# Kernel optimization log

Hardware: AMD Instinct MI355X
Metric: run time of the kernel (lower is better)

The kernel has to match this reference:

```python
import jax, jax.numpy as jnp
import numpy as np
from jax import lax

GRID_N = 80
C_FEAT = 128
HID = 256
NLAYERS = 12


def _make_grid_mesh(n):
    xs = np.linspace(-0.9, 0.9, n, dtype=np.float32)
    X, Y = np.meshgrid(xs, xs, indexing='xy')
    verts = np.stack([X.ravel(), Y.ravel(), np.zeros(n * n, np.float32)], 1)
    idx = np.arange(n * n).reshape(n, n)
    a = idx[:-1, :-1].ravel(); b = idx[:-1, 1:].ravel()
    c = idx[1:, :-1].ravel(); d = idx[1:, 1:].ravel()
    faces = np.concatenate([np.stack([a, b, c], 1), np.stack([b, d, c], 1)], 0)
    return verts, faces.astype(np.int64)


def _edges_and_inv(faces):
    F = faces.shape[0]
    e = np.concatenate([faces[:, [0, 1]], faces[:, [1, 2]], faces[:, [2, 0]]], 0)
    e = np.sort(e, 1)
    edges, inv = np.unique(e, axis=0, return_inverse=True)
    inv = inv.reshape(-1)
    return edges.astype(np.int32), inv[:F], inv[F:2 * F], inv[2 * F:]


def _subdivide_faces(faces, V):
    # new vertex k is midpoint of unique edge k, placed at index V + k
    edges, i01, i12, i20 = _edges_and_inv(faces)
    m01 = V + i01; m12 = V + i12; m20 = V + i20
    v0, v1, v2 = faces[:, 0], faces[:, 1], faces[:, 2]
    nf = np.concatenate([np.stack([v0, m01, m20], 1), np.stack([v1, m12, m01], 1),
                         np.stack([v2, m20, m12], 1), np.stack([m01, m12, m20], 1)], 0)
    return edges, nf


def _topology():
    verts0, f1 = _make_grid_mesh(GRID_N)
    V1 = verts0.shape[0]
    edges1, f2 = _subdivide_faces(f1, V1)
    V2 = V1 + edges1.shape[0]
    edges2, f3 = _subdivide_faces(f2, V2)
    V3 = V2 + edges2.shape[0]
    edges3 = _edges_and_inv(f3)[0]
    return verts0, edges1, edges2, edges3, V3


def _vert_align(feat, verts):
    # feat [C,H,W]; sample bilinearly at vertex (x,y) in [-1,1], align_corners, zero padding
    C, H, W = feat.shape
    fx = (verts[:, 0] + 1.0) * 0.5 * (W - 1)
    fy = (verts[:, 1] + 1.0) * 0.5 * (H - 1)
    x0 = jnp.floor(fx); y0 = jnp.floor(fy)
    wx = fx - x0; wy = fy - y0
    x0i = x0.astype(jnp.int32); y0i = y0.astype(jnp.int32)
    fT = jnp.transpose(feat, (1, 2, 0))  # [H,W,C]

    def samp(yi, xi):
        valid = ((yi >= 0) & (yi < H) & (xi >= 0) & (xi < W)).astype(feat.dtype)
        v = fT[jnp.clip(yi, 0, H - 1), jnp.clip(xi, 0, W - 1)]
        return v * valid[:, None]

    return (samp(y0i, x0i) * ((1 - wy) * (1 - wx))[:, None]
            + samp(y0i, x0i + 1) * ((1 - wy) * wx)[:, None]
            + samp(y0i + 1, x0i) * (wy * (1 - wx))[:, None]
            + samp(y0i + 1, x0i + 1) * (wy * wx)[:, None])


def _gconv(x, e0, e1, w, b):
    # pytorch3d GraphConv: w0(x) + sum_{j in N(i)} w1(x_j), undirected edges
    h0 = x @ w[0] + b[0]
    h1 = x @ w[1] + b[1]
    agg = jnp.zeros_like(h0).at[e0].add(h1[e1]).at[e1].add(h1[e0])
    return h0 + agg


def _stage(feat, edges, w_in, b_in, w_h, b_h, w_out, b_out):
    e0, e1 = edges[:, 0], edges[:, 1]
    x = _gconv(feat, e0, e1, w_in, b_in)

    def body(xc, p):
        return _gconv(xc, e0, e1, p[0], p[1]), None

    x, _ = lax.scan(body, x, (w_h, b_h))
    coords = _gconv(x, e0, e1, w_out, b_out)
    return x, coords


def _subdiv(f, edges):
    # SubdivideMeshes feature/vertex rule: append edge midpoints
    return jnp.concatenate([f, 0.5 * (f[edges[:, 0]] + f[edges[:, 1]])], 0)


def setup_inputs() -> dict:
    key = jax.random.key(0)
    ks = jax.random.split(key, 16)
    verts0, edges1, edges2, edges3, V3 = _topology()

    def pw(k, din, dout, L=None):
        shape = (L, 2, din, dout) if L else (2, din, dout)
        return jax.random.normal(k, shape, dtype=jnp.float32) / np.float32(np.sqrt(7.0 * din))

    din2 = C_FEAT + HID
    inp = {
        'conv64': jax.random.normal(ks[0], (C_FEAT, 56, 56), jnp.float32),
        'conv128': jax.random.normal(ks[1], (C_FEAT, 28, 28), jnp.float32),
        'conv256': jax.random.normal(ks[2], (C_FEAT, 14, 14), jnp.float32),
        'verts0': jnp.asarray(verts0),
        'edges1': jnp.asarray(edges1), 'edges2': jnp.asarray(edges2), 'edges3': jnp.asarray(edges3),
        'w_in1': pw(ks[3], C_FEAT, HID), 'b_in1': jnp.zeros((2, HID), jnp.float32),
        'w_h1': pw(ks[4], HID, HID, NLAYERS), 'b_h1': jnp.zeros((NLAYERS, 2, HID), jnp.float32),
        'w_out1': pw(ks[5], HID, 3), 'b_out1': jnp.zeros((2, 3), jnp.float32),
        'w_in2': pw(ks[6], din2, HID), 'b_in2': jnp.zeros((2, HID), jnp.float32),
        'w_h2': pw(ks[7], HID, HID, NLAYERS), 'b_h2': jnp.zeros((NLAYERS, 2, HID), jnp.float32),
        'w_out2': pw(ks[8], HID, 3), 'b_out2': jnp.zeros((2, 3), jnp.float32),
        'w_in3': pw(ks[9], din2, HID), 'b_in3': jnp.zeros((2, HID), jnp.float32),
        'w_h3': pw(ks[10], HID, HID, NLAYERS), 'b_h3': jnp.zeros((NLAYERS, 2, HID), jnp.float32),
        'w_out3': pw(ks[11], HID, 3), 'b_out3': jnp.zeros((2, 3), jnp.float32),
    }
    return inp


def reference(conv64, conv128, conv256, verts0,
              w_in1, b_in1, w_h1, b_h1, w_out1, b_out1,
              w_in2, b_in2, w_h2, b_h2, w_out2, b_out2,
              w_in3, b_in3, w_h3, b_h3, w_out3, b_out3,
              edges1, edges2, edges3):
    # stage 1: vert_align on conv64 + 14 graph convs -> coords
    x, c1 = _stage(_vert_align(conv64, verts0), edges1, w_in1, b_in1, w_h1, b_h1, w_out1, b_out1)
    v2 = _subdiv(c1, edges1)
    h2 = _subdiv(x, edges1)
    f2 = jnp.concatenate([_vert_align(conv128, v2), h2], 1)
    x, c2 = _stage(f2, edges2, w_in2, b_in2, w_h2, b_h2, w_out2, b_out2)
    v3 = _subdiv(c2, edges2)
    h3 = _subdiv(x, edges2)
    f3 = jnp.concatenate([_vert_align(conv256, v3), h3], 1)
    _, c3 = _stage(f3, edges3, w_in3, b_in3, w_h3, b_h3, w_out3, b_out3)
    return c3
```

## Files before the change

kernel.cpp:

```cpp
#include <hip/hip_runtime.h>
#include <utility>

#define HID 256

typedef __attribute__((ext_vector_type(8))) short bf16x8;
typedef __attribute__((ext_vector_type(4))) float f32x4;
typedef __attribute__((ext_vector_type(4))) unsigned short us4;
typedef __attribute__((ext_vector_type(4))) unsigned uint4v;

constexpr size_t MAXN3 = 100489;
constexpr size_t MAXE3 = 300200;

constexpr size_t OFF_IN1 = 0;
constexpr size_t OFF_IN2 = OFF_IN1 + 2 * 256 * 128;
constexpr size_t OFF_IN3 = OFF_IN2 + 2 * 256 * 384;
constexpr size_t OFF_H1  = OFF_IN3 + 2 * 256 * 384;
constexpr size_t OFF_H2  = OFF_H1 + 24 * 256 * 256;
constexpr size_t OFF_H3  = OFF_H2 + 24 * 256 * 256;
constexpr size_t WT_TOTAL = OFF_H3 + 24 * 256 * 256;

__device__ __attribute__((aligned(16))) unsigned g_A [MAXN3 * 256];
__device__ __attribute__((aligned(16))) unsigned g_B [MAXN3 * 256];
__device__ __attribute__((aligned(16))) unsigned g_G [MAXN3 * 256];
__device__ __attribute__((aligned(16))) unsigned g_D [MAXN3 * 256];
__device__ __attribute__((aligned(16))) unsigned g_VA[MAXN3 * 128];
__device__ float g_C0[MAXN3 * 3];
__device__ float g_C2[MAXN3 * 3];
__device__ float g_Vv[MAXN3 * 3];
__device__ float g_T [56 * 56 * 128];
__device__ __attribute__((aligned(16))) unsigned short g_Wth[WT_TOTAL];
__device__ __attribute__((aligned(16))) unsigned short g_Wtl[WT_TOTAL];
__device__ int g_deg   [MAXN3];
__device__ int g_rowptr[MAXN3 + 1];
__device__ int g_cursor[MAXN3];
__device__ int g_adj   [2 * MAXE3];
__device__ int g_bsum  [128];

__device__ inline float rec(unsigned u) {
  return __uint_as_float(u & 0xffff0000u) + __uint_as_float(u << 16);
}
__device__ inline unsigned pck(float f) {
  unsigned u = __float_as_uint(f);
  unsigned hi = u & 0xffff0000u;
  unsigned lo = __float_as_uint(f - __uint_as_float(hi)) >> 16;
  return hi | (lo & 0xffffu);
}

#define GLOAD16(g, l)                                                       \
  __builtin_amdgcn_global_load_lds(                                        \
      (const __attribute__((address_space(1))) unsigned*)(g),              \
      (__attribute__((address_space(3))) unsigned*)(l), 16, 0, 0)

__global__ __launch_bounds__(256) void k_wtrans(const float* __restrict__ W,
                                                unsigned short* __restrict__ Oh,
                                                unsigned short* __restrict__ Ol,
                                                int K) {
  __shared__ float Ls[64][65];
  int ktb = blockIdx.x, cb = blockIdx.y, mat = blockIdx.z;
  int nktb = gridDim.x;
  const float* Wm = W + (size_t)mat * K * 256;
  int t = threadIdx.x;
#pragma unroll
  for (int i = 0; i < 16; ++i) {
    int idx = i * 256 + t;
    int kk = idx >> 6, cc = idx & 63;
    Ls[kk][cc] = Wm[(size_t)(ktb * 64 + kk) * 256 + cb * 64 + cc];
  }
  __syncthreads();
  size_t tb = ((size_t)(mat * 4 + cb) * nktb + ktb) * 4096;
#pragma unroll
  for (int i = 0; i < 2; ++i) {
    int c = t * 2 + i;
    int n = c >> 3, sp = c & 7;
    int kbase = (sp ^ (n & 7)) * 8;
    unsigned short hb[8], lb[8];
#pragma unroll
    for (int j = 0; j < 8; ++j) {
      float v = Ls[kbase + j][n];
      unsigned u = __float_as_uint(v);
      unsigned short hi = (unsigned short)(u >> 16);
      float hf = __uint_as_float(u & 0xffff0000u);
      hb[j] = hi;
      lb[j] = (unsigned short)(__float_as_uint(v - hf) >> 16);
    }
    *(us4*)(Oh + tb + c * 8)     = (us4){hb[0], hb[1], hb[2], hb[3]};
    *(us4*)(Oh + tb + c * 8 + 4) = (us4){hb[4], hb[5], hb[6], hb[7]};
    *(us4*)(Ol + tb + c * 8)     = (us4){lb[0], lb[1], lb[2], lb[3]};
    *(us4*)(Ol + tb + c * 8 + 4) = (us4){lb[4], lb[5], lb[6], lb[7]};
  }
}


__global__ __launch_bounds__(256) void k_count(const int* __restrict__ edges,
                                               int* __restrict__ deg, int E) {
  int e = blockIdx.x * blockDim.x + threadIdx.x;
  if (e >= E) return;
  atomicAdd(&deg[edges[2 * e + 0]], 1);
  atomicAdd(&deg[edges[2 * e + 1]], 1);
}

__global__ __launch_bounds__(256) void k_scan_part(const int* __restrict__ deg,
                                                   int* __restrict__ bsum, int N) {
  __shared__ int s[256];
  int t = threadIdx.x;
  int base = blockIdx.x * 1024 + t * 4;
  int v = 0;
#pragma unroll
  for (int i = 0; i < 4; ++i) {
    int idx = base + i;
    if (idx < N) v += deg[idx];
  }
  s[t] = v;
  __syncthreads();
  for (int off = 128; off > 0; off >>= 1) {
    if (t < off) s[t] += s[t + off];
    __syncthreads();
  }
  if (t == 0) bsum[blockIdx.x] = s[0];
}

__global__ __launch_bounds__(128) void k_scan_top(int* __restrict__ bsum, int nb) {
  __shared__ int s[128];
  int t = threadIdx.x;
  s[t] = (t < nb) ? bsum[t] : 0;
  __syncthreads();
  for (int off = 1; off < 128; off <<= 1) {
    int v = (t >= off) ? s[t - off] : 0;
    __syncthreads();
    s[t] += v;
    __syncthreads();
  }
  if (t < nb) bsum[t] = (t == 0) ? 0 : s[t - 1];
}

__global__ __launch_bounds__(256) void k_scan_write(const int* __restrict__ deg,
                                                    const int* __restrict__ bsum,
                                                    int* __restrict__ rowptr,
                                                    int* __restrict__ cursor, int N) {
  __shared__ int s[256];
  int t = threadIdx.x;
  int base = blockIdx.x * 1024;
  int d[4];
  int local = 0;
#pragma unroll
  for (int i = 0; i < 4; ++i) {
    int idx = base + t * 4 + i;
    d[i] = (idx < N) ? deg[idx] : 0;
    local += d[i];
  }
  s[t] = local;
  __syncthreads();
  for (int off = 1; off < 256; off <<= 1) {
    int v = (t >= off) ? s[t - off] : 0;
    __syncthreads();
    s[t] += v;
    __syncthreads();
  }
  int run = bsum[blockIdx.x] + s[t] - local;
#pragma unroll
  for (int i = 0; i < 4; ++i) {
    int idx = base + t * 4 + i;
    if (idx < N) {
      rowptr[idx] = run;
      cursor[idx] = run;
    }
    run += d[i];
  }
  if (blockIdx.x == gridDim.x - 1 && t == 255) rowptr[N] = run;
}

__global__ __launch_bounds__(256) void k_fill(const int* __restrict__ edges,
                                              int* __restrict__ cursor,
                                              int* __restrict__ adj, int E) {
  int e = blockIdx.x * blockDim.x + threadIdx.x;
  if (e >= E) return;
  int a = edges[2 * e + 0];
  int b = edges[2 * e + 1];
  adj[atomicAdd(&cursor[a], 1)] = b;
  adj[atomicAdd(&cursor[b], 1)] = a;
}


__global__ __launch_bounds__(128) void k_transpose(const float* __restrict__ in,
                                                   float* __restrict__ out, int HW) {
  int p = blockIdx.x;
  int c = threadIdx.x;
  if (p < HW) out[(size_t)p * 128 + c] = in[(size_t)c * HW + p];
}

__global__ __launch_bounds__(128) void k_vert_align(const float* __restrict__ fT,
                                                    const float* __restrict__ verts,
                                                    unsigned* __restrict__ out,
                                                    int N, int H, int W) {
  int v = blockIdx.x;
  if (v >= N) return;
  int c = threadIdx.x;
  float vx = verts[(size_t)v * 3 + 0];
  float vy = verts[(size_t)v * 3 + 1];
  float fx = (vx + 1.f) * 0.5f * (float)(W - 1);
  float fy = (vy + 1.f) * 0.5f * (float)(H - 1);
  float x0f = floorf(fx), y0f = floorf(fy);
  float wx = fx - x0f, wy = fy - y0f;
  int x0 = (int)x0f, y0 = (int)y0f;
  float acc = 0.f;
#pragma unroll
  for (int dy = 0; dy < 2; ++dy) {
#pragma unroll
    for (int dx = 0; dx < 2; ++dx) {
      int yi = y0 + dy, xi = x0 + dx;
      bool valid = (yi >= 0) && (yi < H) && (xi >= 0) && (xi < W);
      int yc = min(max(yi, 0), H - 1);
      int xc = min(max(xi, 0), W - 1);
      float val = fT[((size_t)yc * W + xc) * 128 + c];
      float wgt = (dy ? wy : 1.f - wy) * (dx ? wx : 1.f - wx);
      acc += valid ? val * wgt : 0.f;
    }
  }
  out[(size_t)v * 128 + c] = pck(acc);
}

template <int CH>
__global__ __launch_bounds__(256) void k_gather(const int* __restrict__ rowptr,
                                                const int* __restrict__ adj,
                                                const unsigned* __restrict__ X,
                                                unsigned* __restrict__ G, int N) {
  int idx = blockIdx.x * blockDim.x + threadIdx.x;
  int v = idx / (CH / 4);
  if (v >= N) return;
  int c = (idx % (CH / 4)) * 4;
  float a0 = 0.f, a1 = 0.f, a2 = 0.f, a3 = 0.f;
  int lo = rowptr[v], hi = rowptr[v + 1];
  for (int i = lo; i < hi; ++i) {
    uint4 h = *(const uint4*)(X + (size_t)adj[i] * CH + c);
    a0 += rec(h.x); a1 += rec(h.y); a2 += rec(h.z); a3 += rec(h.w);
  }
  uint4 o;
  o.x = pck(a0); o.y = pck(a1); o.z = pck(a2); o.w = pck(a3);
  *(uint4*)(G + (size_t)v * CH + c) = o;
}

struct Panels {
  const unsigned* p[4];
  int ks[4];
  int ld[4];
};

#define SWZ(row, slot) (((row) * 64) + (((slot) ^ ((row) & 7)) * 8))

__device__ inline bf16x8 as_bf(uint4v v) {
  union { uint4v u; bf16x8 b; } x;
  x.u = v;
  return x.b;
}

__global__ __launch_bounds__(256) void k_layer(
    Panels pd, int Kmm,
    const unsigned short* __restrict__ w0h, const unsigned short* __restrict__ w0l,
    const unsigned short* __restrict__ w1h, const unsigned short* __restrict__ w1l,
    int Kw,
    const float* __restrict__ b0, const float* __restrict__ b1,
    const int* __restrict__ deg,
    unsigned* __restrict__ Y, int N) {
  __shared__ __attribute__((aligned(16))) unsigned X_lds[128 * 64];
  __shared__ __attribute__((aligned(16))) unsigned short Wh_lds[4096];
  __shared__ __attribute__((aligned(16))) unsigned short Wl_lds[4096];
  int tid = threadIdx.x;
  int lane = tid & 63;
  int wid = tid >> 6;
  int wm = wid & 1, wn = wid >> 1;

  int nrt = (N + 127) >> 7;
  int total = nrt * 4;
  int flat = blockIdx.x;
  int rowtile, colblk;
  if ((flat & ~31) + 32 <= total) {
    int sub = flat & 31;
    rowtile = (flat >> 5) * 8 + (sub & 7);
    colblk = sub >> 3;
  } else {
    rowtile = flat >> 2;
    colblk = flat & 3;
  }
  int row0 = rowtile * 128;
  int col0 = colblk * 64;
  int nktbw = Kw >> 6;

  f32x4 acc[4][2];
#pragma unroll
  for (int m = 0; m < 4; ++m)
#pragma unroll
    for (int n = 0; n < 2; ++n) acc[m][n] = (f32x4){0.f, 0.f, 0.f, 0.f};

  for (int kt = 0; kt < Kmm; kt += 64) {
    int pi = (kt >= pd.ks[1]) + (kt >= pd.ks[2]) + (kt >= pd.ks[3]);
    const unsigned* base = pd.p[pi];
    int ld = pd.ld[pi];
    int koff = kt - pd.ks[pi];
#pragma unroll
    for (int i = 0; i < 8; ++i) {
      int inst = wid * 8 + i;
      int row = inst * 4 + (lane >> 4);
      int j = lane & 15;
      int vc = min(row0 + row, N - 1);
      const unsigned* src = base + (size_t)vc * ld + koff + ((j ^ (row & 15)) << 2);
      GLOAD16(src, &X_lds[inst * 256]);
    }
    const unsigned short* th;
    const unsigned short* tl;
    {
      int ktb = (kt < Kw) ? (kt >> 6) : ((kt - Kw) >> 6);
      const unsigned short* mh = (kt < Kw) ? w0h : w1h;
      const unsigned short* ml = (kt < Kw) ? w0l : w1l;
      size_t tb = ((size_t)(colblk * nktbw + ktb)) * 4096;
      th = mh + tb;
      tl = ml + tb;
    }
#pragma unroll
    for (int i = 0; i < 2; ++i) {
      int inst = wid * 2 + i;
      GLOAD16(th + inst * 512 + lane * 8, &Wh_lds[inst * 512]);
      GLOAD16(tl + inst * 512 + lane * 8, &Wl_lds[inst * 512]);
    }
    __syncthreads();
#pragma unroll
    for (int ks = 0; ks < 2; ++ks) {
      int slot = ks * 4 + (lane >> 4);
      bf16x8 ah[4], al[4];
#pragma unroll
      for (int m = 0; m < 4; ++m) {
        int row = wm * 64 + m * 16 + (lane & 15);
        int rx = row & 15;
        const unsigned* xp = X_lds + row * 64;
        uint4 u0 = *(const uint4*)(xp + (((2 * slot) ^ rx) << 2));
        uint4 u1 = *(const uint4*)(xp + (((2 * slot + 1) ^ rx) << 2));
        uint4v hv, lv;
        hv.x = __builtin_amdgcn_perm(u0.y, u0.x, 0x07060302u);
        hv.y = __builtin_amdgcn_perm(u0.w, u0.z, 0x07060302u);
        hv.z = __builtin_amdgcn_perm(u1.y, u1.x, 0x07060302u);
        hv.w = __builtin_amdgcn_perm(u1.w, u1.z, 0x07060302u);
        lv.x = __builtin_amdgcn_perm(u0.y, u0.x, 0x05040100u);
        lv.y = __builtin_amdgcn_perm(u0.w, u0.z, 0x05040100u);
        lv.z = __builtin_amdgcn_perm(u1.y, u1.x, 0x05040100u);
        lv.w = __builtin_amdgcn_perm(u1.w, u1.z, 0x05040100u);
        ah[m] = as_bf(hv);
        al[m] = as_bf(lv);
      }
      bf16x8 bh[2], bl[2];
#pragma unroll
      for (int n = 0; n < 2; ++n) {
        int nr = wn * 32 + n * 16 + (lane & 15);
        int wi = SWZ(nr, slot);
        bh[n] = *(const bf16x8*)&Wh_lds[wi];
        bl[n] = *(const bf16x8*)&Wl_lds[wi];
      }
#pragma unroll
      for (int m = 0; m < 4; ++m)
#pragma unroll
        for (int n = 0; n < 2; ++n) {
          f32x4 c = acc[m][n];
          c = __builtin_amdgcn_mfma_f32_16x16x32_bf16(al[m], bh[n], c, 0, 0, 0);
          c = __builtin_amdgcn_mfma_f32_16x16x32_bf16(ah[m], bl[n], c, 0, 0, 0);
          c = __builtin_amdgcn_mfma_f32_16x16x32_bf16(ah[m], bh[n], c, 0, 0, 0);
          acc[m][n] = c;
        }
    }
    __syncthreads();
  }

#pragma unroll
  for (int m = 0; m < 4; ++m) {
    int rbase = row0 + wm * 64 + m * 16 + (lane >> 4) * 4;
    float dv[4];
#pragma unroll
    for (int r = 0; r < 4; ++r)
      dv[r] = (rbase + r < N) ? (float)deg[rbase + r] : 0.f;
#pragma unroll
    for (int n = 0; n < 2; ++n) {
      int col = col0 + wn * 32 + n * 16 + (lane & 15);
      float bb0 = b0[col], bb1 = b1[col];
      f32x4 v = acc[m][n];
#pragma unroll
      for (int r = 0; r < 4; ++r) {
        int row = rbase + r;
        if (row < N)
          Y[(size_t)row * HID + col] = pck(v[r] + bb0 + dv[r] * bb1);
      }
    }
  }
}

__global__ __launch_bounds__(256) void k_rowdot6(const unsigned* __restrict__ X,
                                                 const float* __restrict__ W,
                                                 const float* __restrict__ b,
                                                 float* __restrict__ Y0,
                                                 float* __restrict__ Y1, int N) {
  int gid = blockIdx.x * blockDim.x + threadIdx.x;
  int row = gid >> 6;
  int lane = threadIdx.x & 63;
  if (row >= N) return;
  uint4 xv = ((const uint4*)(X + (size_t)row * HID))[lane];
  float s[6] = {0.f, 0.f, 0.f, 0.f, 0.f, 0.f};
#pragma unroll
  for (int k = 0; k < 4; ++k) {
    float x = rec((&xv.x)[k]);
    int kk = lane * 4 + k;
#pragma unroll
    for (int j = 0; j < 3; ++j) {
      s[j]     += x * W[kk * 3 + j];
      s[3 + j] += x * W[768 + kk * 3 + j];
    }
  }
#pragma unroll
  for (int off = 32; off > 0; off >>= 1)
#pragma unroll
    for (int j = 0; j < 6; ++j) s[j] += __shfl_down(s[j], off);
  if (lane == 0) {
#pragma unroll
    for (int j = 0; j < 3; ++j) {
      Y0[(size_t)row * 3 + j] = s[j] + b[j];
      Y1[(size_t)row * 3 + j] = s[3 + j] + b[3 + j];
    }
  }
}

__global__ __launch_bounds__(256) void k_scatter3(const int* __restrict__ edges,
                                                  const float* __restrict__ H,
                                                  float* __restrict__ OUT, int E) {
  int e = blockIdx.x * blockDim.x + threadIdx.x;
  if (e >= E) return;
  int a = edges[(size_t)e * 2 + 0];
  int b = edges[(size_t)e * 2 + 1];
#pragma unroll
  for (int k = 0; k < 3; ++k) {
    atomicAdd(&OUT[(size_t)a * 3 + k], H[(size_t)b * 3 + k]);
    atomicAdd(&OUT[(size_t)b * 3 + k], H[(size_t)a * 3 + k]);
  }
}

__global__ __launch_bounds__(256) void k_subdiv3(const float* __restrict__ c,
                                                 const int* __restrict__ edges,
                                                 float* __restrict__ v, int N, int E) {
  int i = blockIdx.x * blockDim.x + threadIdx.x;
  if (i >= N + E) return;
  if (i < N) {
#pragma unroll
    for (int k = 0; k < 3; ++k) v[(size_t)i * 3 + k] = c[(size_t)i * 3 + k];
  } else {
    int e = i - N;
    int a = edges[(size_t)e * 2 + 0];
    int b = edges[(size_t)e * 2 + 1];
#pragma unroll
    for (int k = 0; k < 3; ++k)
      v[(size_t)i * 3 + k] = 0.5f * (c[(size_t)a * 3 + k] + c[(size_t)b * 3 + k]);
  }
}

__global__ __launch_bounds__(256) void k_subdiv_feat(const unsigned* __restrict__ x,
                                                     const int* __restrict__ edges,
                                                     unsigned* __restrict__ out, int N, int E) {
  int idx = blockIdx.x * blockDim.x + threadIdx.x;
  int v = idx >> 6;
  if (v >= N + E) return;
  int c = (threadIdx.x & 63) * 4;
  uint4 r;
  if (v < N) {
    r = *(const uint4*)(x + (size_t)v * HID + c);
  } else {
    int e = v - N;
    int a = edges[(size_t)e * 2 + 0];
    int b = edges[(size_t)e * 2 + 1];
    uint4 xa = *(const uint4*)(x + (size_t)a * HID + c);
    uint4 xb = *(const uint4*)(x + (size_t)b * HID + c);
    r.x = pck(0.5f * (rec(xa.x) + rec(xb.x)));
    r.y = pck(0.5f * (rec(xa.y) + rec(xb.y)));
    r.z = pck(0.5f * (rec(xa.z) + rec(xb.z)));
    r.w = pck(0.5f * (rec(xa.w) + rec(xb.w)));
  }
  *(uint4*)(out + (size_t)v * HID + c) = r;
}


extern "C" void kernel_launch(void* const* d_in, const int* in_sizes, int n_in,
                              void* d_out, int out_size, void* d_ws, size_t ws_size,
                              hipStream_t stream) {
  const float* conv64  = (const float*)d_in[0];
  const float* conv128 = (const float*)d_in[1];
  const float* conv256 = (const float*)d_in[2];
  const float* verts0  = (const float*)d_in[3];
  const int*   edges1  = (const int*)d_in[4];
  const int*   edges2  = (const int*)d_in[5];
  const int*   edges3  = (const int*)d_in[6];
  const float* w_in1 = (const float*)d_in[7],  *b_in1 = (const float*)d_in[8];
  const float* w_h1  = (const float*)d_in[9],  *b_h1  = (const float*)d_in[10];
  const float* w_out1= (const float*)d_in[11], *b_out1= (const float*)d_in[12];
  const float* w_in2 = (const float*)d_in[13], *b_in2 = (const float*)d_in[14];
  const float* w_h2  = (const float*)d_in[15], *b_h2  = (const float*)d_in[16];
  const float* w_out2= (const float*)d_in[17], *b_out2= (const float*)d_in[18];
  const float* w_in3 = (const float*)d_in[19], *b_in3 = (const float*)d_in[20];
  const float* w_h3  = (const float*)d_in[21], *b_h3  = (const float*)d_in[22];
  const float* w_out3= (const float*)d_in[23], *b_out3= (const float*)d_in[24];

  const int N1 = in_sizes[3] / 3;
  const int E1 = in_sizes[4] / 2;
  const int E2 = in_sizes[5] / 2;
  const int E3 = in_sizes[6] / 2;
  const int N2 = N1 + E1;
  const int N3 = N2 + E2;
  if ((size_t)N3 > MAXN3 || (size_t)E3 > MAXE3) return;

  unsigned *A, *B, *G, *D, *VA;
  float *C0, *C2, *Vv, *T;
  unsigned short *Wth, *Wtl;
  int *deg, *rowptr, *cursor, *adj, *bsum;
  hipGetSymbolAddress((void**)&A,  HIP_SYMBOL(g_A));
  hipGetSymbolAddress((void**)&B,  HIP_SYMBOL(g_B));
  hipGetSymbolAddress((void**)&G,  HIP_SYMBOL(g_G));
  hipGetSymbolAddress((void**)&D,  HIP_SYMBOL(g_D));
  hipGetSymbolAddress((void**)&VA, HIP_SYMBOL(g_VA));
  hipGetSymbolAddress((void**)&C0, HIP_SYMBOL(g_C0));
  hipGetSymbolAddress((void**)&C2, HIP_SYMBOL(g_C2));
  hipGetSymbolAddress((void**)&Vv, HIP_SYMBOL(g_Vv));
  hipGetSymbolAddress((void**)&T,  HIP_SYMBOL(g_T));
  hipGetSymbolAddress((void**)&Wth, HIP_SYMBOL(g_Wth));
  hipGetSymbolAddress((void**)&Wtl, HIP_SYMBOL(g_Wtl));
  hipGetSymbolAddress((void**)&deg,    HIP_SYMBOL(g_deg));
  hipGetSymbolAddress((void**)&rowptr, HIP_SYMBOL(g_rowptr));
  hipGetSymbolAddress((void**)&cursor, HIP_SYMBOL(g_cursor));
  hipGetSymbolAddress((void**)&adj,    HIP_SYMBOL(g_adj));
  hipGetSymbolAddress((void**)&bsum,   HIP_SYMBOL(g_bsum));

  k_wtrans<<<dim3(2, 4, 2),  256, 0, stream>>>(w_in1, Wth + OFF_IN1, Wtl + OFF_IN1, 128);
  k_wtrans<<<dim3(6, 4, 2),  256, 0, stream>>>(w_in2, Wth + OFF_IN2, Wtl + OFF_IN2, 384);
  k_wtrans<<<dim3(6, 4, 2),  256, 0, stream>>>(w_in3, Wth + OFF_IN3, Wtl + OFF_IN3, 384);
  k_wtrans<<<dim3(4, 4, 24), 256, 0, stream>>>(w_h1,  Wth + OFF_H1,  Wtl + OFF_H1,  256);
  k_wtrans<<<dim3(4, 4, 24), 256, 0, stream>>>(w_h2,  Wth + OFF_H2,  Wtl + OFF_H2,  256);
  k_wtrans<<<dim3(4, 4, 24), 256, 0, stream>>>(w_h3,  Wth + OFF_H3,  Wtl + OFF_H3,  256);

  const int BIG = 0x7fffffff;

  auto layerGrid = [](int N) { return dim3((unsigned)(((N + 127) / 128) * 4)); };

  auto build_csr = [&](const int* edges, int E, int N) {
    hipMemsetAsync(deg, 0, (size_t)N * sizeof(int), stream);
    k_count<<<(E + 255) / 256, 256, 0, stream>>>(edges, deg, E);
    int nb = (N + 1023) / 1024;
    k_scan_part<<<nb, 256, 0, stream>>>(deg, bsum, N);
    k_scan_top<<<1, 128, 0, stream>>>(bsum, nb);
    k_scan_write<<<nb, 256, 0, stream>>>(deg, bsum, rowptr, cursor, N);
    k_fill<<<(E + 255) / 256, 256, 0, stream>>>(edges, cursor, adj, E);
  };

  auto gconv_hidden = [&](size_t offH, const float* bh, int N) {
    unsigned* X = A; unsigned* Y = B;
    for (int l = 0; l < 12; ++l) {
      const unsigned short* w0h = Wth + offH + (size_t)(2 * l + 0) * 65536;
      const unsigned short* w0l = Wtl + offH + (size_t)(2 * l + 0) * 65536;
      const unsigned short* w1h = Wth + offH + (size_t)(2 * l + 1) * 65536;
      const unsigned short* w1l = Wtl + offH + (size_t)(2 * l + 1) * 65536;
      const float* b0 = bh + (size_t)l * 2 * HID;
      const float* b1 = b0 + HID;
      k_gather<256><<<((size_t)N * 64 + 255) / 256, 256, 0, stream>>>(rowptr, adj, X, G, N);
      Panels pd = {{X, G, nullptr, nullptr}, {0, 256, BIG, BIG}, {256, 256, 0, 0}};
      k_layer<<<layerGrid(N), 256, 0, stream>>>(pd, 512, w0h, w0l, w1h, w1l, 256,
                                                b0, b1, deg, Y, N);
      std::swap(X, Y);
    }
  };

  auto gconv_out = [&](const unsigned* X, const float* wo, const float* bo,
                       float* Cdst, const int* edges, int E, int N) {
    k_rowdot6<<<((size_t)N * 64 + 255) / 256, 256, 0, stream>>>(X, wo, bo, Cdst, C2, N);
    k_scatter3<<<(E + 255) / 256, 256, 0, stream>>>(edges, C2, Cdst, E);
  };

  build_csr(edges1, E1, N1);
  k_transpose<<<56 * 56, 128, 0, stream>>>(conv64, T, 56 * 56);
  k_vert_align<<<N1, 128, 0, stream>>>(T, verts0, VA, N1, 56, 56);
  k_gather<128><<<((size_t)N1 * 32 + 255) / 256, 256, 0, stream>>>(rowptr, adj, VA, G, N1);
  {
    Panels pd = {{VA, G, nullptr, nullptr}, {0, 128, BIG, BIG}, {128, 128, 0, 0}};
    k_layer<<<layerGrid(N1), 256, 0, stream>>>(pd, 256,
        Wth + OFF_IN1, Wtl + OFF_IN1, Wth + OFF_IN1 + 32768, Wtl + OFF_IN1 + 32768, 128,
        b_in1, b_in1 + HID, deg, A, N1);
  }
  gconv_hidden(OFF_H1, b_h1, N1);
  gconv_out(A, w_out1, b_out1, C0, edges1, E1, N1);
  k_subdiv3<<<(N2 + 255) / 256, 256, 0, stream>>>(C0, edges1, Vv, N1, E1);
  k_subdiv_feat<<<((size_t)N2 * 64 + 255) / 256, 256, 0, stream>>>(A, edges1, D, N1, E1);

  build_csr(edges2, E2, N2);
  k_transpose<<<28 * 28, 128, 0, stream>>>(conv128, T, 28 * 28);
  k_vert_align<<<N2, 128, 0, stream>>>(T, Vv, VA, N2, 28, 28);
  k_gather<128><<<((size_t)N2 * 32 + 255) / 256, 256, 0, stream>>>(rowptr, adj, VA, G, N2);
  k_gather<256><<<((size_t)N2 * 64 + 255) / 256, 256, 0, stream>>>(rowptr, adj, D, B, N2);
  {
    const size_t m0 = OFF_IN2, m1 = OFF_IN2 + (size_t)256 * 384;
    Panels pd = {{VA, D, G, B}, {0, 128, 384, 512}, {128, 256, 128, 256}};
    k_layer<<<layerGrid(N2), 256, 0, stream>>>(pd, 768,
        Wth + m0, Wtl + m0, Wth + m1, Wtl + m1, 384,
        b_in2, b_in2 + HID, deg, A, N2);
  }
  gconv_hidden(OFF_H2, b_h2, N2);
  gconv_out(A, w_out2, b_out2, C0, edges2, E2, N2);
  k_subdiv3<<<(N3 + 255) / 256, 256, 0, stream>>>(C0, edges2, Vv, N2, E2);
  k_subdiv_feat<<<((size_t)N3 * 64 + 255) / 256, 256, 0, stream>>>(A, edges2, D, N2, E2);

  build_csr(edges3, E3, N3);
  k_transpose<<<14 * 14, 128, 0, stream>>>(conv256, T, 14 * 14);
  k_vert_align<<<N3, 128, 0, stream>>>(T, Vv, VA, N3, 14, 14);
  k_gather<128><<<((size_t)N3 * 32 + 255) / 256, 256, 0, stream>>>(rowptr, adj, VA, G, N3);
  k_gather<256><<<((size_t)N3 * 64 + 255) / 256, 256, 0, stream>>>(rowptr, adj, D, B, N3);
  {
    const size_t m0 = OFF_IN3, m1 = OFF_IN3 + (size_t)256 * 384;
    Panels pd = {{VA, D, G, B}, {0, 128, 384, 512}, {128, 256, 128, 256}};
    k_layer<<<layerGrid(N3), 256, 0, stream>>>(pd, 768,
        Wth + m0, Wtl + m0, Wth + m1, Wtl + m1, 384,
        b_in3, b_in3 + HID, deg, A, N3);
  }
  gconv_hidden(OFF_H3, b_h3, N3);
  float* OUT = (float*)d_out;
  k_rowdot6<<<((size_t)N3 * 64 + 255) / 256, 256, 0, stream>>>(A, w_out3, b_out3, OUT, C2, N3);
  k_scatter3<<<(E3 + 255) / 256, 256, 0, stream>>>(edges3, C2, OUT, E3);
}
```

Measured before the change: 4.577 ms.

## Store activations as separate bf16 hi/lo planes instead of interleaved words

Activation buffers used to hold packed 32-bit words (bf16 hi and lo halves interleaved). They are now split into two separate planes of unsigned short, across the gather, vert_align, subdivision, rowdot and layer kernels. In the GEMM kernel this removes the per-fragment perm instructions that de-interleaved hi and lo from LDS, since each plane can be loaded directly as a bf16x8 operand. The cost is twice as many global and LDS load streams per tile and separate write streams in every producer kernel, with the same total byte traffic.

Measured after the change: 4.221 ms. 7.8% less time.

```diff
diff --git a/kernel.cpp b/kernel.cpp
--- a/kernel.cpp
+++ b/kernel.cpp
@@ -6,7 +6,7 @@
 typedef __attribute__((ext_vector_type(8))) short bf16x8;
 typedef __attribute__((ext_vector_type(4))) float f32x4;
 typedef __attribute__((ext_vector_type(4))) unsigned short us4;
-typedef __attribute__((ext_vector_type(4))) unsigned uint4v;
+typedef __attribute__((ext_vector_type(8))) unsigned short us8;
 
 constexpr size_t MAXN3 = 100489;
 constexpr size_t MAXE3 = 300200;
@@ -19,11 +19,16 @@
 constexpr size_t OFF_H3  = OFF_H2 + 24 * 256 * 256;
 constexpr size_t WT_TOTAL = OFF_H3 + 24 * 256 * 256;
 
-__device__ __attribute__((aligned(16))) unsigned g_A [MAXN3 * 256];
-__device__ __attribute__((aligned(16))) unsigned g_B [MAXN3 * 256];
-__device__ __attribute__((aligned(16))) unsigned g_G [MAXN3 * 256];
-__device__ __attribute__((aligned(16))) unsigned g_D [MAXN3 * 256];
-__device__ __attribute__((aligned(16))) unsigned g_VA[MAXN3 * 128];
+__device__ __attribute__((aligned(16))) unsigned short g_Ah[MAXN3 * 256];
+__device__ __attribute__((aligned(16))) unsigned short g_Al[MAXN3 * 256];
+__device__ __attribute__((aligned(16))) unsigned short g_Bh[MAXN3 * 256];
+__device__ __attribute__((aligned(16))) unsigned short g_Bl[MAXN3 * 256];
+__device__ __attribute__((aligned(16))) unsigned short g_Gh[MAXN3 * 256];
+__device__ __attribute__((aligned(16))) unsigned short g_Gl[MAXN3 * 256];
+__device__ __attribute__((aligned(16))) unsigned short g_Dh[MAXN3 * 256];
+__device__ __attribute__((aligned(16))) unsigned short g_Dl[MAXN3 * 256];
+__device__ __attribute__((aligned(16))) unsigned short g_VAh[MAXN3 * 128];
+__device__ __attribute__((aligned(16))) unsigned short g_VAl[MAXN3 * 128];
 __device__ float g_C0[MAXN3 * 3];
 __device__ float g_C2[MAXN3 * 3];
 __device__ float g_Vv[MAXN3 * 3];
@@ -36,20 +41,20 @@
 __device__ int g_adj   [2 * MAXE3];
 __device__ int g_bsum  [128];
 
-__device__ inline float rec(unsigned u) {
-  return __uint_as_float(u & 0xffff0000u) + __uint_as_float(u << 16);
-}
-__device__ inline unsigned pck(float f) {
+__device__ inline float b2f(unsigned short h) {
+  return __uint_as_float((unsigned)h << 16);
+}
+__device__ inline void fsplit(float f, unsigned short& h, unsigned short& l) {
   unsigned u = __float_as_uint(f);
-  unsigned hi = u & 0xffff0000u;
-  unsigned lo = __float_as_uint(f - __uint_as_float(hi)) >> 16;
-  return hi | (lo & 0xffffu);
+  h = (unsigned short)(u >> 16);
+  float hf = __uint_as_float(u & 0xffff0000u);
+  l = (unsigned short)(__float_as_uint(f - hf) >> 16);
 }
 
 #define GLOAD16(g, l)                                                       \
   __builtin_amdgcn_global_load_lds(                                        \
-      (const __attribute__((address_space(1))) unsigned*)(g),              \
-      (__attribute__((address_space(3))) unsigned*)(l), 16, 0, 0)
+      (const __attribute__((address_space(1))) unsigned*)(const void*)(g), \
+      (__attribute__((address_space(3))) unsigned*)(void*)(l), 16, 0, 0)
 
 __global__ __launch_bounds__(256) void k_wtrans(const float* __restrict__ W,
                                                 unsigned short* __restrict__ Oh,
@@ -77,11 +82,10 @@
 #pragma unroll
     for (int j = 0; j < 8; ++j) {
       float v = Ls[kbase + j][n];
-      unsigned u = __float_as_uint(v);
-      unsigned short hi = (unsigned short)(u >> 16);
-      float hf = __uint_as_float(u & 0xffff0000u);
+      unsigned short hi, lo;
+      fsplit(v, hi, lo);
       hb[j] = hi;
-      lb[j] = (unsigned short)(__float_as_uint(v - hf) >> 16);
+      lb[j] = lo;
     }
     *(us4*)(Oh + tb + c * 8)     = (us4){hb[0], hb[1], hb[2], hb[3]};
     *(us4*)(Oh + tb + c * 8 + 4) = (us4){hb[4], hb[5], hb[6], hb[7]};
@@ -190,7 +194,8 @@
 
 __global__ __launch_bounds__(128) void k_vert_align(const float* __restrict__ fT,
                                                     const float* __restrict__ verts,
-                                                    unsigned* __restrict__ out,
+                                                    unsigned short* __restrict__ oh,
+                                                    unsigned short* __restrict__ ol,
                                                     int N, int H, int W) {
   int v = blockIdx.x;
   if (v >= N) return;
@@ -216,42 +221,53 @@
       acc += valid ? val * wgt : 0.f;
     }
   }
-  out[(size_t)v * 128 + c] = pck(acc);
+  unsigned short h, l;
+  fsplit(acc, h, l);
+  oh[(size_t)v * 128 + c] = h;
+  ol[(size_t)v * 128 + c] = l;
 }
 
 template <int CH>
 __global__ __launch_bounds__(256) void k_gather(const int* __restrict__ rowptr,
                                                 const int* __restrict__ adj,
-                                                const unsigned* __restrict__ X,
-                                                unsigned* __restrict__ G, int N) {
+                                                const unsigned short* __restrict__ Xh,
+                                                const unsigned short* __restrict__ Xl,
+                                                unsigned short* __restrict__ Gh,
+                                                unsigned short* __restrict__ Gl, int N) {
+  constexpr int TPV = CH / 8;
   int idx = blockIdx.x * blockDim.x + threadIdx.x;
-  int v = idx / (CH / 4);
+  int v = idx / TPV;
   if (v >= N) return;
-  int c = (idx % (CH / 4)) * 4;
-  float a0 = 0.f, a1 = 0.f, a2 = 0.f, a3 = 0.f;
+  int c = (idx % TPV) * 8;
+  float a[8] = {};
   int lo = rowptr[v], hi = rowptr[v + 1];
   for (int i = lo; i < hi; ++i) {
-    uint4 h = *(const uint4*)(X + (size_t)adj[i] * CH + c);
-    a0 += rec(h.x); a1 += rec(h.y); a2 += rec(h.z); a3 += rec(h.w);
-  }
-  uint4 o;
-  o.x = pck(a0); o.y = pck(a1); o.z = pck(a2); o.w = pck(a3);
-  *(uint4*)(G + (size_t)v * CH + c) = o;
+    size_t base = (size_t)adj[i] * CH + c;
+    us8 h = *(const us8*)(Xh + base);
+    us8 l = *(const us8*)(Xl + base);
+#pragma unroll
+    for (int j = 0; j < 8; ++j) a[j] += b2f(h[j]) + b2f(l[j]);
+  }
+  us8 oh, ol;
+#pragma unroll
+  for (int j = 0; j < 8; ++j) {
+    unsigned short hh, ll;
+    fsplit(a[j], hh, ll);
+    oh[j] = hh;
+    ol[j] = ll;
+  }
+  *(us8*)(Gh + (size_t)v * CH + c) = oh;
+  *(us8*)(Gl + (size_t)v * CH + c) = ol;
 }
 
 struct Panels {
-  const unsigned* p[4];
+  const unsigned short* ph[4];
+  const unsigned short* pl[4];
   int ks[4];
   int ld[4];
 };
 
-#define SWZ(row, slot) (((row) * 64) + (((slot) ^ ((row) & 7)) * 8))
-
-__device__ inline bf16x8 as_bf(uint4v v) {
-  union { uint4v u; bf16x8 b; } x;
-  x.u = v;
-  return x.b;
-}
+#define SWZ(row, slot) (((row) * 64) + (((slot) ^ ((row) & 7)) << 3))
 
 __global__ __launch_bounds__(256) void k_layer(
     Panels pd, int Kmm,
@@ -260,8 +276,9 @@
     int Kw,
     const float* __restrict__ b0, const float* __restrict__ b1,
     const int* __restrict__ deg,
-    unsigned* __restrict__ Y, int N) {
-  __shared__ __attribute__((aligned(16))) unsigned X_lds[128 * 64];
+    unsigned short* __restrict__ Yh, unsigned short* __restrict__ Yl, int N) {
+  __shared__ __attribute__((aligned(16))) unsigned short Xh_lds[128 * 64];
+  __shared__ __attribute__((aligned(16))) unsigned short Xl_lds[128 * 64];
   __shared__ __attribute__((aligned(16))) unsigned short Wh_lds[4096];
   __shared__ __attribute__((aligned(16))) unsigned short Wl_lds[4096];
   int tid = threadIdx.x;
@@ -293,17 +310,18 @@
 
   for (int kt = 0; kt < Kmm; kt += 64) {
     int pi = (kt >= pd.ks[1]) + (kt >= pd.ks[2]) + (kt >= pd.ks[3]);
-    const unsigned* base = pd.p[pi];
+    const unsigned short* bph = pd.ph[pi];
+    const unsigned short* bpl = pd.pl[pi];
     int ld = pd.ld[pi];
     int koff = kt - pd.ks[pi];
 #pragma unroll
-    for (int i = 0; i < 8; ++i) {
-      int inst = wid * 8 + i;
-      int row = inst * 4 + (lane >> 4);
-      int j = lane & 15;
-      int vc = min(row0 + row, N - 1);
-      const unsigned* src = base + (size_t)vc * ld + koff + ((j ^ (row & 15)) << 2);
-      GLOAD16(src, &X_lds[inst * 256]);
+    for (int i = 0; i < 4; ++i) {
+      int c = (wid * 4 + i) * 64 + lane;
+      int row = c >> 3, slot = c & 7;
+      int vg = min(row0 + row, N - 1);
+      size_t srcoff = (size_t)vg * ld + koff + ((slot ^ (row & 7)) << 3);
+      GLOAD16(bph + srcoff, &Xh_lds[(size_t)c * 8]);
+      GLOAD16(bpl + srcoff, &Xl_lds[(size_t)c * 8]);
     }
     const unsigned short* th;
     const unsigned short* tl;
@@ -329,21 +347,9 @@
 #pragma unroll
       for (int m = 0; m < 4; ++m) {
         int row = wm * 64 + m * 16 + (lane & 15);
-        int rx = row & 15;
-        const unsigned* xp = X_lds + row * 64;
-        uint4 u0 = *(const uint4*)(xp + (((2 * slot) ^ rx) << 2));
-        uint4 u1 = *(const uint4*)(xp + (((2 * slot + 1) ^ rx) << 2));
-        uint4v hv, lv;
-        hv.x = __builtin_amdgcn_perm(u0.y, u0.x, 0x07060302u);
-        hv.y = __builtin_amdgcn_perm(u0.w, u0.z, 0x07060302u);
-        hv.z = __builtin_amdgcn_perm(u1.y, u1.x, 0x07060302u);
-        hv.w = __builtin_amdgcn_perm(u1.w, u1.z, 0x07060302u);
-        lv.x = __builtin_amdgcn_perm(u0.y, u0.x, 0x05040100u);
-        lv.y = __builtin_amdgcn_perm(u0.w, u0.z, 0x05040100u);
-        lv.z = __builtin_amdgcn_perm(u1.y, u1.x, 0x05040100u);
-        lv.w = __builtin_amdgcn_perm(u1.w, u1.z, 0x05040100u);
-        ah[m] = as_bf(hv);
-        al[m] = as_bf(lv);
+        int off = SWZ(row, slot);
+        ah[m] = *(const bf16x8*)&Xh_lds[off];
+        al[m] = *(const bf16x8*)&Xl_lds[off];
       }
       bf16x8 bh[2], bl[2];
 #pragma unroll
@@ -382,14 +388,19 @@
 #pragma unroll
       for (int r = 0; r < 4; ++r) {
         int row = rbase + r;
-        if (row < N)
-          Y[(size_t)row * HID + col] = pck(v[r] + bb0 + dv[r] * bb1);
+        if (row < N) {
+          unsigned short h, l;
+          fsplit(v[r] + bb0 + dv[r] * bb1, h, l);
+          Yh[(size_t)row * HID + col] = h;
+          Yl[(size_t)row * HID + col] = l;
+        }
       }
     }
   }
 }
 
-__global__ __launch_bounds__(256) void k_rowdot6(const unsigned* __restrict__ X,
+__global__ __launch_bounds__(256) void k_rowdot6(const unsigned short* __restrict__ Xh,
+                                                 const unsigned short* __restrict__ Xl,
                                                  const float* __restrict__ W,
                                                  const float* __restrict__ b,
                                                  float* __restrict__ Y0,
@@ -398,11 +409,13 @@
   int row = gid >> 6;
   int lane = threadIdx.x & 63;
   if (row >= N) return;
-  uint4 xv = ((const uint4*)(X + (size_t)row * HID))[lane];
+  size_t base = (size_t)row * HID + lane * 4;
+  us4 hv = *(const us4*)(Xh + base);
+  us4 lv = *(const us4*)(Xl + base);
   float s[6] = {0.f, 0.f, 0.f, 0.f, 0.f, 0.f};
 #pragma unroll
   for (int k = 0; k < 4; ++k) {
-    float x = rec((&xv.x)[k]);
+    float x = b2f(hv[k]) + b2f(lv[k]);
     int kk = lane * 4 + k;
 #pragma unroll
     for (int j = 0; j < 3; ++j) {
@@ -455,28 +468,39 @@
   }
 }
 
-__global__ __launch_bounds__(256) void k_subdiv_feat(const unsigned* __restrict__ x,
+__global__ __launch_bounds__(256) void k_subdiv_feat(const unsigned short* __restrict__ xh,
+                                                     const unsigned short* __restrict__ xl,
                                                      const int* __restrict__ edges,
-                                                     unsigned* __restrict__ out, int N, int E) {
+                                                     unsigned short* __restrict__ oh,
+                                                     unsigned short* __restrict__ ol,
+                                                     int N, int E) {
   int idx = blockIdx.x * blockDim.x + threadIdx.x;
-  int v = idx >> 6;
+  int v = idx >> 5;
   if (v >= N + E) return;
-  int c = (threadIdx.x & 63) * 4;
-  uint4 r;
+  int c = (idx & 31) * 8;
+  us8 rh, rl;
   if (v < N) {
-    r = *(const uint4*)(x + (size_t)v * HID + c);
+    rh = *(const us8*)(xh + (size_t)v * HID + c);
+    rl = *(const us8*)(xl + (size_t)v * HID + c);
   } else {
     int e = v - N;
     int a = edges[(size_t)e * 2 + 0];
     int b = edges[(size_t)e * 2 + 1];
-    uint4 xa = *(const uint4*)(x + (size_t)a * HID + c);
-    uint4 xb = *(const uint4*)(x + (size_t)b * HID + c);
-    r.x = pck(0.5f * (rec(xa.x) + rec(xb.x)));
-    r.y = pck(0.5f * (rec(xa.y) + rec(xb.y)));
-    r.z = pck(0.5f * (rec(xa.z) + rec(xb.z)));
-    r.w = pck(0.5f * (rec(xa.w) + rec(xb.w)));
-  }
-  *(uint4*)(out + (size_t)v * HID + c) = r;
+    us8 ahv = *(const us8*)(xh + (size_t)a * HID + c);
+    us8 alv = *(const us8*)(xl + (size_t)a * HID + c);
+    us8 bhv = *(const us8*)(xh + (size_t)b * HID + c);
+    us8 blv = *(const us8*)(xl + (size_t)b * HID + c);
+#pragma unroll
+    for (int j = 0; j < 8; ++j) {
+      float f = 0.5f * ((b2f(ahv[j]) + b2f(alv[j])) + (b2f(bhv[j]) + b2f(blv[j])));
+      unsigned short hh, ll;
+      fsplit(f, hh, ll);
+      rh[j] = hh;
+      rl[j] = ll;
+    }
+  }
+  *(us8*)(oh + (size_t)v * HID + c) = rh;
+  *(us8*)(ol + (size_t)v * HID + c) = rl;
 }
 
 
@@ -508,15 +532,20 @@
   const int N3 = N2 + E2;
   if ((size_t)N3 > MAXN3 || (size_t)E3 > MAXE3) return;
 
-  unsigned *A, *B, *G, *D, *VA;
+  unsigned short *Ah, *Al, *Bh, *Bl, *Gh, *Gl, *Dh, *Dl, *VAh, *VAl;
   float *C0, *C2, *Vv, *T;
   unsigned short *Wth, *Wtl;
   int *deg, *rowptr, *cursor, *adj, *bsum;
-  hipGetSymbolAddress((void**)&A,  HIP_SYMBOL(g_A));
-  hipGetSymbolAddress((void**)&B,  HIP_SYMBOL(g_B));
-  hipGetSymbolAddress((void**)&G,  HIP_SYMBOL(g_G));
-  hipGetSymbolAddress((void**)&D,  HIP_SYMBOL(g_D));
-  hipGetSymbolAddress((void**)&VA, HIP_SYMBOL(g_VA));
+  hipGetSymbolAddress((void**)&Ah,  HIP_SYMBOL(g_Ah));
+  hipGetSymbolAddress((void**)&Al,  HIP_SYMBOL(g_Al));
+  hipGetSymbolAddress((void**)&Bh,  HIP_SYMBOL(g_Bh));
+  hipGetSymbolAddress((void**)&Bl,  HIP_SYMBOL(g_Bl));
+  hipGetSymbolAddress((void**)&Gh,  HIP_SYMBOL(g_Gh));
+  hipGetSymbolAddress((void**)&Gl,  HIP_SYMBOL(g_Gl));
+  hipGetSymbolAddress((void**)&Dh,  HIP_SYMBOL(g_Dh));
+  hipGetSymbolAddress((void**)&Dl,  HIP_SYMBOL(g_Dl));
+  hipGetSymbolAddress((void**)&VAh, HIP_SYMBOL(g_VAh));
+  hipGetSymbolAddress((void**)&VAl, HIP_SYMBOL(g_VAl));
   hipGetSymbolAddress((void**)&C0, HIP_SYMBOL(g_C0));
   hipGetSymbolAddress((void**)&C2, HIP_SYMBOL(g_C2));
   hipGetSymbolAddress((void**)&Vv, HIP_SYMBOL(g_Vv));
@@ -551,7 +580,7 @@
   };
 
   auto gconv_hidden = [&](size_t offH, const float* bh, int N) {
-    unsigned* X = A; unsigned* Y = B;
+    unsigned short *Xh = Ah, *Xl = Al, *Yh = Bh, *Yl = Bl;
     for (int l = 0; l < 12; ++l) {
       const unsigned short* w0h = Wth + offH + (size_t)(2 * l + 0) * 65536;
       const unsigned short* w0l = Wtl + offH + (size_t)(2 * l + 0) * 65536;
@@ -559,66 +588,81 @@
       const unsigned short* w1l = Wtl + offH + (size_t)(2 * l + 1) * 65536;
       const float* b0 = bh + (size_t)l * 2 * HID;
       const float* b1 = b0 + HID;
-      k_gather<256><<<((size_t)N * 64 + 255) / 256, 256, 0, stream>>>(rowptr, adj, X, G, N);
-      Panels pd = {{X, G, nullptr, nullptr}, {0, 256, BIG, BIG}, {256, 256, 0, 0}};
+      k_gather<256><<<((size_t)N * 32 + 255) / 256, 256, 0, stream>>>(
+          rowptr, adj, Xh, Xl, Gh, Gl, N);
+      Panels pd = {{Xh, Gh, nullptr, nullptr}, {Xl, Gl, nullptr, nullptr},
+                   {0, 256, BIG, BIG}, {256, 256, 0, 0}};
       k_layer<<<layerGrid(N), 256, 0, stream>>>(pd, 512, w0h, w0l, w1h, w1l, 256,
-                                                b0, b1, deg, Y, N);
-      std::swap(X, Y);
+                                                b0, b1, deg, Yh, Yl, N);
+      std::swap(Xh, Yh);
+      std::swap(Xl, Yl);
     }
   };
 
-  auto gconv_out = [&](const unsigned* X, const float* wo, const float* bo,
+  auto gconv_out = [&](const unsigned short* Xh, const unsigned short* Xl,
+                       const float* wo, const float* bo,
                        float* Cdst, const int* edges, int E, int N) {
-    k_rowdot6<<<((size_t)N * 64 + 255) / 256, 256, 0, stream>>>(X, wo, bo, Cdst, C2, N);
+    k_rowdot6<<<((size_t)N * 64 + 255) / 256, 256, 0, stream>>>(Xh, Xl, wo, bo, Cdst, C2, N);
     k_scatter3<<<(E + 255) / 256, 256, 0, stream>>>(edges, C2, Cdst, E);
   };
 
   build_csr(edges1, E1, N1);
   k_transpose<<<56 * 56, 128, 0, stream>>>(conv64, T, 56 * 56);
-  k_vert_align<<<N1, 128, 0, stream>>>(T, verts0, VA, N1, 56, 56);
-  k_gather<128><<<((size_t)N1 * 32 + 255) / 256, 256, 0, stream>>>(rowptr, adj, VA, G, N1);
+  k_vert_align<<<N1, 128, 0, stream>>>(T, verts0, VAh, VAl, N1, 56, 56);
+  k_gather<128><<<((size_t)N1 * 16 + 255) / 256, 256, 0, stream>>>(
+      rowptr, adj, VAh, VAl, Gh, Gl, N1);
   {
-    Panels pd = {{VA, G, nullptr, nullptr}, {0, 128, BIG, BIG}, {128, 128, 0, 0}};
+    Panels pd = {{VAh, Gh, nullptr, nullptr}, {VAl, Gl, nullptr, nullptr},
+                 {0, 128, BIG, BIG}, {128, 128, 0, 0}};
     k_layer<<<layerGrid(N1), 256, 0, stream>>>(pd, 256,
         Wth + OFF_IN1, Wtl + OFF_IN1, Wth + OFF_IN1 + 32768, Wtl + OFF_IN1 + 32768, 128,
-        b_in1, b_in1 + HID, deg, A, N1);
+        b_in1, b_in1 + HID, deg, Ah, Al, N1);
   }
   gconv_hidden(OFF_H1, b_h1, N1);
-  gconv_out(A, w_out1, b_out1, C0, edges1, E1, N1);
+  gconv_out(Ah, Al, w_out1, b_out1, C0, edges1, E1, N1);
   k_subdiv3<<<(N2 + 255) / 256, 256, 0, stream>>>(C0, edges1, Vv, N1, E1);
-  k_subdiv_feat<<<((size_t)N2 * 64 + 255) / 256, 256, 0, stream>>>(A, edges1, D, N1, E1);
+  k_subdiv_feat<<<((size_t)N2 * 32 + 255) / 256, 256, 0, stream>>>(
+      Ah, Al, edges1, Dh, Dl, N1, E1);
 
   build_csr(edges2, E2, N2);
   k_transpose<<<28 * 28, 128, 0, stream>>>(conv128, T, 28 * 28);
-  k_vert_align<<<N2, 128, 0, stream>>>(T, Vv, VA, N2, 28, 28);
-  k_gather<128><<<((size_t)N2 * 32 + 255) / 256, 256, 0, stream>>>(rowptr, adj, VA, G, N2);
-  k_gather<256><<<((size_t)N2 * 64 + 255) / 256, 256, 0, stream>>>(rowptr, adj, D, B, N2);
+  k_vert_align<<<N2, 128, 0, stream>>>(T, Vv, VAh, VAl, N2, 28, 28);
+  k_gather<128><<<((size_t)N2 * 16 + 255) / 256, 256, 0, stream>>>(
+      rowptr, adj, VAh, VAl, Gh, Gl, N2);
+  k_gather<256><<<((size_t)N2 * 32 + 255) / 256, 256, 0, stream>>>(
+      rowptr, adj, Dh, Dl, Bh, Bl, N2);
   {
     const size_t m0 = OFF_IN2, m1 = OFF_IN2 + (size_t)256 * 384;
-    Panels pd = {{VA, D, G, B}, {0, 128, 384, 512}, {128, 256, 128, 256}};
+    Panels pd = {{VAh, Dh, Gh, Bh}, {VAl, Dl, Gl, Bl},
+                 {0, 128, 384, 512}, {128, 256, 128, 256}};
     k_layer<<<layerGrid(N2), 256, 0, stream>>>(pd, 768,
         Wth + m0, Wtl + m0, Wth + m1, Wtl + m1, 384,
-        b_in2, b_in2 + HID, deg, A, N2);
+        b_in2, b_in2 + HID, deg, Ah, Al, N2);
   }
   gconv_hidden(OFF_H2, b_h2, N2);
-  gconv_out(A, w_out2, b_out2, C0, edges2, E2, N2);
+  gconv_out(Ah, Al, w_out2, b_out2, C0, edges2, E2, N2);
   k_subdiv3<<<(N3 + 255) / 256, 256, 0, stream>>>(C0, edges2, Vv, N2, E2);
-  k_subdiv_feat<<<((size_t)N3 * 64 + 255) / 256, 256, 0, stream>>>(A, edges2, D, N2, E2);
+  k_subdiv_feat<<<((size_t)N3 * 32 + 255) / 256, 256, 0, stream>>>(
+      Ah, Al, edges2, Dh, Dl, N2, E2);
 
   build_csr(edges3, E3, N3);
   k_transpose<<<14 * 14, 128, 0, stream>>>(conv256, T, 14 * 14);
-  k_vert_align<<<N3, 128, 0, stream>>>(T, Vv, VA, N3, 14, 14);
-  k_gather<128><<<((size_t)N3 * 32 + 255) / 256, 256, 0, stream>>>(rowptr, adj, VA, G, N3);
-  k_gather<256><<<((size_t)N3 * 64 + 255) / 256, 256, 0, stream>>>(rowptr, adj, D, B, N3);
+  k_vert_align<<<N3, 128, 0, stream>>>(T, Vv, VAh, VAl, N3, 14, 14);
+  k_gather<128><<<((size_t)N3 * 16 + 255) / 256, 256, 0, stream>>>(
+      rowptr, adj, VAh, VAl, Gh, Gl, N3);
+  k_gather<256><<<((size_t)N3 * 32 + 255) / 256, 256, 0, stream>>>(
+      rowptr, adj, Dh, Dl, Bh, Bl, N3);
   {
     const size_t m0 = OFF_IN3, m1 = OFF_IN3 + (size_t)256 * 384;
-    Panels pd = {{VA, D, G, B}, {0, 128, 384, 512}, {128, 256, 128, 256}};
+    Panels pd = {{VAh, Dh, Gh, Bh}, {VAl, Dl, Gl, Bl},
+                 {0, 128, 384, 512}, {128, 256, 128, 256}};
     k_layer<<<layerGrid(N3), 256, 0, stream>>>(pd, 768,
         Wth + m0, Wtl + m0, Wth + m1, Wtl + m1, 384,
-        b_in3, b_in3 + HID, deg, A, N3);
+        b_in3, b_in3 + HID, deg, Ah, Al, N3);
   }
   gconv_hidden(OFF_H3, b_h3, N3);
   float* OUT = (float*)d_out;
-  k_rowdot6<<<((size_t)N3 * 64 + 255) / 256, 256, 0, stream>>>(A, w_out3, b_out3, OUT, C2, N3);
+  k_rowdot6<<<((size_t)N3 * 64 + 255) / 256, 256, 0, stream>>>(
+      Ah, Al, w_out3, b_out3, OUT, C2, N3);
   k_scatter3<<<(E3 + 255) / 256, 256, 0, stream>>>(edges3, C2, OUT, E3);
 }
```
